# Kernel tuning notes

Measured on AMD Instinct MI355X. Metric: run time of the kernel, lower is better.

The kernel has to match this reference:

```python
import jax, jax.numpy as jnp
import numpy as np


def setup_inputs() -> dict:
    key = jax.random.key(0)
    k1, k2 = jax.random.split(key)
    x = jax.random.normal(k1, (4, 1, 16384), dtype=jnp.float32)  # [B, C, T]
    # dictionary initialized uniform(-1, 1) as in nn.Parameter(...).uniform_(-1, 1)
    d = jax.random.uniform(k2, (256, 1, 256), dtype=jnp.float32, minval=-1.0, maxval=1.0)  # [A, C, K]
    return {"x": x, "d": d, "n_iterations": 16}


def reference(x, d, n_iterations):
    B, C, T = x.shape
    A, _, K = d.shape
    pad = K // 2
    # normalize each atom over (channels, atom_size) dims, i.e. d_normalization_dims=(-1,-2)
    norms = jnp.linalg.norm(d.reshape(A, -1), axis=-1)
    dn = d / (norms[:, None, None] + 1e-12)

    # work in a padded domain so conv output position == start index in padded residual
    rp = jnp.pad(x, ((0, 0), (0, 0), (pad, pad)))        # residual, [B, C, T+2*pad]
    recon = jnp.zeros_like(rp)                            # accumulated reconstruction
    Tout = T + 2 * pad - K + 1                            # conv output length

    def step(carry, _):
        rp, recon = carry
        # cross-correlation of residual with every atom: [B, A, Tout]
        fm = jax.lax.conv_general_dilated(
            rp, dn, window_strides=(1,), padding='VALID',
            dimension_numbers=('NCH', 'OIH', 'NCH'))
        flat = fm.reshape(B, A * Tout)
        idx = jnp.argmax(flat, axis=-1)                   # signed max, per batch item
        val = jnp.take_along_axis(flat, idx[:, None], axis=-1)[:, 0]
        atom_idx = idx // Tout
        pos = idx % Tout                                  # start index in padded domain
        atoms = dn[atom_idx] * val[:, None, None]         # [B, C, K]

        def upd(r, rec, a, p):
            seg = jax.lax.dynamic_slice(r, (0, p), (C, K))
            r2 = jax.lax.dynamic_update_slice(r, seg - a, (0, p))
            segr = jax.lax.dynamic_slice(rec, (0, p), (C, K))
            rec2 = jax.lax.dynamic_update_slice(rec, segr + a, (0, p))
            return r2, rec2

        rp2, recon2 = jax.vmap(upd)(rp, recon, atoms, pos)
        return (rp2, recon2), None

    (rp, recon), _ = jax.lax.scan(step, (rp, recon), None, length=n_iterations)
    # crop padding -> reconstruction with same shape as x
    return recon[:, :, pad:pad + T]
```

## Files before the change

### kernel.cpp

```cpp
#include <hip/hip_runtime.h>
#include <hip/hip_cooperative_groups.h>
#include <math.h>

namespace cg = cooperative_groups;

#define B    4
#define T    16384
#define A    256
#define K    256
#define PAD  128
#define TP   (T + 2*PAD)
#define TOUT (TP - K + 1)
#define ITERS 16
#define CHUNK 512
#define NCHUNK 33
#define NCP  36
#define TILE 2048
#define NTILE 9
#define NBLK 512

struct Smem {
    float rp[TILE + K + 16];
    float dnA[K];
    float dnB[K];
    float dnsel[K];
    float wv[16]; int wi[16];
    float fv; int fi;
};

#define TAP(acc, s0,s1,s2,s3, dq) { acc = fmaf(s0,(dq).x,acc); acc = fmaf(s1,(dq).y,acc); \
                                    acc = fmaf(s2,(dq).z,acc); acc = fmaf(s3,(dq).w,acc); }

__device__ __forceinline__ void wave_amax(float& bv, int& bi) {
    #pragma unroll
    for (int off = 32; off; off >>= 1) {
        float ov = __shfl_down(bv, off);
        int   oi = __shfl_down(bi, off);
        if (ov > bv || (ov == bv && oi < bi)) { bv = ov; bi = oi; }
    }
}

__device__ __forceinline__ void gbar(unsigned* c, unsigned target) {
    __syncthreads();
    if (threadIdx.x == 0) {
        __hip_atomic_fetch_add(c, 1u, __ATOMIC_RELEASE, __HIP_MEMORY_SCOPE_AGENT);
        while (__hip_atomic_load(c, __ATOMIC_ACQUIRE, __HIP_MEMORY_SCOPE_AGENT) < target)
            __builtin_amdgcn_s_sleep(2);
    }
    __syncthreads();
}

__device__ __forceinline__ void dev_norm(int bid, int tid, const float* __restrict__ d,
                                         float* __restrict__ dn, Smem& sm) {
    if (bid < 128) {
        int lane = tid & 63, w = tid >> 6;
        #pragma unroll
        for (int s = 0; s < 2; s++) {
            int atom = (bid & 127)*2 + s;
            float v = d[atom*K + tid];
            float sq = v*v;
            #pragma unroll
            for (int off = 32; off; off >>= 1) sq += __shfl_down(sq, off);
            if (lane == 0) sm.wv[w] = sq;
            __syncthreads();
            float norm = sqrtf(sm.wv[0] + sm.wv[1] + sm.wv[2] + sm.wv[3]) + 1e-12f;
            dn[atom*K + tid] = v / norm;
            __syncthreads();
        }
    }
}

__device__ __forceinline__ void dev_init(int bid, int tid, const float* __restrict__ x,
                                         float* __restrict__ rp, float* __restrict__ recon) {
    for (int i = bid*256 + tid; i < B*TP; i += NBLK*256) {
        int bb = i / TP, t = i - bb*TP;
        float v = (t >= PAD && t < PAD + T) ? x[bb*T + (t - PAD)] : 0.f;
        rp[i] = v;
        recon[i] = 0.f;
    }
}

__device__ void dev_conv(int a0, int b, int tid, const float* __restrict__ rp,
                         const float* __restrict__ dn,
                         float* __restrict__ segval, int* __restrict__ segidx,
                         float* __restrict__ abv, int* __restrict__ abi, Smem& sm) {
    const int aA = a0*2, aB = a0*2 + 1;
    const int lane = tid & 63, w = tid >> 6;
    sm.dnA[tid] = dn[aA*K + tid];
    sm.dnB[tid] = dn[aB*K + tid];
    const float4* rp4 = (const float4*)(rp + (size_t)b*TP);

    for (int tile = 0; tile < NTILE; tile++) {
        int t0 = tile * TILE;
        __syncthreads();
        float4* s4 = (float4*)sm.rp;
        for (int i = tid; i < 580; i += 256) {
            int g = t0/4 + i;
            float4 v = {0.f,0.f,0.f,0.f};
            if (g*4 < TP) v = rp4[g];
            s4[i] = v;
        }
        __syncthreads();
        const float4* srp4 = (const float4*)sm.rp;
        const float4* dA4  = (const float4*)sm.dnA;
        const float4* dB4  = (const float4*)sm.dnB;
        float accA0[4] = {0,0,0,0}, accA1[4] = {0,0,0,0};
        float accB0[4] = {0,0,0,0}, accB1[4] = {0,0,0,0};
        float4 p = srp4[tid];
        float4 q = srp4[tid + 256];
        #pragma unroll 4
        for (int kq = 0; kq < 64; kq++) {
            float4 dA = dA4[kq];
            float4 dB = dB4[kq];
            float4 pn = srp4[tid + kq + 1];
            float4 qn = srp4[tid + 256 + kq + 1];
            TAP(accA0[0], p.x,p.y,p.z,p.w, dA); TAP(accA0[1], p.y,p.z,p.w,pn.x, dA);
            TAP(accA0[2], p.z,p.w,pn.x,pn.y, dA); TAP(accA0[3], p.w,pn.x,pn.y,pn.z, dA);
            TAP(accB0[0], p.x,p.y,p.z,p.w, dB); TAP(accB0[1], p.y,p.z,p.w,pn.x, dB);
            TAP(accB0[2], p.z,p.w,pn.x,pn.y, dB); TAP(accB0[3], p.w,pn.x,pn.y,pn.z, dB);
            TAP(accA1[0], q.x,q.y,q.z,q.w, dA); TAP(accA1[1], q.y,q.z,q.w,qn.x, dA);
            TAP(accA1[2], q.z,q.w,qn.x,qn.y, dA); TAP(accA1[3], q.w,qn.x,qn.y,qn.z, dA);
            TAP(accB1[0], q.x,q.y,q.z,q.w, dB); TAP(accB1[1], q.y,q.z,q.w,qn.x, dB);
            TAP(accB1[2], q.z,q.w,qn.x,qn.y, dB); TAP(accB1[3], q.w,qn.x,qn.y,qn.z, dB);
            p = pn; q = qn;
        }
        int lt = tid * 4;
        float bvA0 = -INFINITY, bvA1 = -INFINITY, bvB0 = -INFINITY, bvB1 = -INFINITY;
        int biA0 = 0x7fffffff, biA1 = 0x7fffffff, biB0 = 0x7fffffff, biB1 = 0x7fffffff;
        #pragma unroll
        for (int j = 0; j < 4; j++) {
            int t = t0 + lt + j;
            if (t < TOUT) {
                if (accA0[j] > bvA0) { bvA0 = accA0[j]; biA0 = aA*TOUT + t; }
                if (accB0[j] > bvB0) { bvB0 = accB0[j]; biB0 = aB*TOUT + t; }
            }
            int t1 = t0 + 1024 + lt + j;
            if (t1 < TOUT) {
                if (accA1[j] > bvA1) { bvA1 = accA1[j]; biA1 = aA*TOUT + t1; }
                if (accB1[j] > bvB1) { bvB1 = accB1[j]; biB1 = aB*TOUT + t1; }
            }
        }
        wave_amax(bvA0, biA0); wave_amax(bvA1, biA1);
        wave_amax(bvB0, biB0); wave_amax(bvB1, biB1);
        if (lane == 0) {
            sm.wv[w]    = bvA0; sm.wi[w]    = biA0;
            sm.wv[4+w]  = bvA1; sm.wi[4+w]  = biA1;
            sm.wv[8+w]  = bvB0; sm.wi[8+w]  = biB0;
            sm.wv[12+w] = bvB1; sm.wi[12+w] = biB1;
        }
        __syncthreads();
        if (tid < 4) {
            float v0 = sm.wv[2*tid];   int i0 = sm.wi[2*tid];
            float v1 = sm.wv[2*tid+1]; int i1 = sm.wi[2*tid+1];
            if (v1 > v0 || (v1 == v0 && i1 < i0)) { v0 = v1; i0 = i1; }
            int chunk = tile*4 + tid;
            if (chunk < NCHUNK) {
                segval[((size_t)b*A + aA)*NCP + chunk] = v0;
                segidx[((size_t)b*A + aA)*NCP + chunk] = i0;
            }
        } else if (tid >= 64 && tid < 68) {
            int c = tid - 64;
            float v0 = sm.wv[8+2*c];   int i0 = sm.wi[8+2*c];
            float v1 = sm.wv[8+2*c+1]; int i1 = sm.wi[8+2*c+1];
            if (v1 > v0 || (v1 == v0 && i1 < i0)) { v0 = v1; i0 = i1; }
            int chunk = tile*4 + c;
            if (chunk < NCHUNK) {
                segval[((size_t)b*A + aB)*NCP + chunk] = v0;
                segidx[((size_t)b*A + aB)*NCP + chunk] = i0;
            }
        }
    }
    __syncthreads();
    if (w < 2) {
        int atom = (w == 0) ? aA : aB;
        float bv = -INFINITY; int bi = 0x7fffffff;
        if (lane < NCHUNK) {
            bv = segval[((size_t)b*A + atom)*NCP + lane];
            bi = segidx[((size_t)b*A + atom)*NCP + lane];
        }
        wave_amax(bv, bi);
        if (lane == 0) { abv[b*A + atom] = bv; abi[b*A + atom] = bi; }
    }
}

__device__ void dev_iter(int a0, int b, int tid, int last,
                         const float* __restrict__ avc, const int* __restrict__ aic,
                         float* __restrict__ avn, int* __restrict__ ain,
                         const float* __restrict__ rin, float* __restrict__ rout,
                         float* __restrict__ recon, const float* __restrict__ dn,
                         float* __restrict__ segval, int* __restrict__ segidx, Smem& sm) {
    const int aA = a0*2, aB = a0*2 + 1;
    const int lane = tid & 63, w = tid >> 6;
    sm.dnA[tid] = dn[aA*K + tid];
    sm.dnB[tid] = dn[aB*K + tid];
    {
        float bv = avc[b*A + tid]; int bi = aic[b*A + tid];
        wave_amax(bv, bi);
        if (lane == 0) { sm.wv[w] = bv; sm.wi[w] = bi; }
        __syncthreads();
        if (tid == 0) {
            bv = sm.wv[0]; bi = sm.wi[0];
            for (int j = 1; j < 4; j++)
                if (sm.wv[j] > bv || (sm.wv[j] == bv && sm.wi[j] < bi)) { bv = sm.wv[j]; bi = sm.wi[j]; }
            sm.fv = bv; sm.fi = bi;
        }
        __syncthreads();
    }
    float val = sm.fv; int idx = sm.fi;
    int atom = idx / TOUT, pos = idx - atom*TOUT;
    sm.dnsel[tid] = dn[atom*K + tid];

    int lo = pos - (K-1); if (lo < 0) lo = 0;
    int c_lo = lo >> 9;
    int tbase = c_lo * CHUNK;

    if (!last) {
        const float4* rin4 = (const float4*)(rin + (size_t)b*TP);
        float4* s4 = (float4*)sm.rp;
        for (int i = tid; i < 324; i += 256) {
            int g = tbase/4 + i;
            float4 v = {0.f,0.f,0.f,0.f};
            if (g*4 < TP) v = rin4[g];
            s4[i] = v;
        }
    }
    __syncthreads();
    if (!last) {
        const float4* rin4 = (const float4*)(rin + (size_t)b*TP);
        float4* rout4 = (float4*)(rout + (size_t)b*TP);
        int i = a0*256 + tid;
        if (i < TP/4) {
            float4 v = rin4[i];
            int o = i*4 - pos;
            if (o > -4 && o < K) {
                if (o+0 >= 0 && o+0 < K) v.x -= val * sm.dnsel[o+0];
                if (o+1 >= 0 && o+1 < K) v.y -= val * sm.dnsel[o+1];
                if (o+2 >= 0 && o+2 < K) v.z -= val * sm.dnsel[o+2];
                if (o+3 >= 0 && o+3 < K) v.w -= val * sm.dnsel[o+3];
            }
            rout4[i] = v;
        }
    }
    if (a0 == 0) {
        recon[(size_t)b*TP + pos + tid] += val * sm.dnsel[tid];
    }
    if (last) return;

    sm.rp[pos + tid - tbase] -= val * sm.dnsel[tid];
    __syncthreads();

    const float4* srp4 = (const float4*)sm.rp;
    const float4* dA4  = (const float4*)sm.dnA;
    const float4* dB4  = (const float4*)sm.dnB;
    float cA[4] = {0,0,0,0}, cB[4] = {0,0,0,0};
    float4 p = srp4[tid];
    #pragma unroll 4
    for (int kq = 0; kq < 64; kq++) {
        float4 dA = dA4[kq];
        float4 dB = dB4[kq];
        float4 pn = srp4[tid + kq + 1];
        TAP(cA[0], p.x,p.y,p.z,p.w, dA); TAP(cA[1], p.y,p.z,p.w,pn.x, dA);
        TAP(cA[2], p.z,p.w,pn.x,pn.y, dA); TAP(cA[3], p.w,pn.x,pn.y,pn.z, dA);
        TAP(cB[0], p.x,p.y,p.z,p.w, dB); TAP(cB[1], p.y,p.z,p.w,pn.x, dB);
        TAP(cB[2], p.z,p.w,pn.x,pn.y, dB); TAP(cB[3], p.w,pn.x,pn.y,pn.z, dB);
        p = pn;
    }
    int lt = tid * 4;
    float bvA = -INFINITY, bvB = -INFINITY;
    int biA = 0x7fffffff, biB = 0x7fffffff;
    #pragma unroll
    for (int j = 0; j < 4; j++) {
        int t = tbase + lt + j;
        if (t < TOUT) {
            if (cA[j] > bvA) { bvA = cA[j]; biA = aA*TOUT + t; }
            if (cB[j] > bvB) { bvB = cB[j]; biB = aB*TOUT + t; }
        }
    }
    wave_amax(bvA, biA); wave_amax(bvB, biB);
    if (lane == 0) { sm.wv[w] = bvA; sm.wi[w] = biA; sm.wv[8+w] = bvB; sm.wi[8+w] = biB; }
    __syncthreads();
    if (tid < 2) {
        float v0 = sm.wv[2*tid];   int i0 = sm.wi[2*tid];
        float v1 = sm.wv[2*tid+1]; int i1 = sm.wi[2*tid+1];
        if (v1 > v0 || (v1 == v0 && i1 < i0)) { v0 = v1; i0 = i1; }
        int chunk = c_lo + tid;
        if (chunk < NCHUNK) {
            segval[((size_t)b*A + aA)*NCP + chunk] = v0;
            segidx[((size_t)b*A + aA)*NCP + chunk] = i0;
        }
    } else if (tid >= 64 && tid < 66) {
        int c = tid - 64;
        float v0 = sm.wv[8+2*c];   int i0 = sm.wi[8+2*c];
        float v1 = sm.wv[8+2*c+1]; int i1 = sm.wi[8+2*c+1];
        if (v1 > v0 || (v1 == v0 && i1 < i0)) { v0 = v1; i0 = i1; }
        int chunk = c_lo + c;
        if (chunk < NCHUNK) {
            segval[((size_t)b*A + aB)*NCP + chunk] = v0;
            segidx[((size_t)b*A + aB)*NCP + chunk] = i0;
        }
    }
    __syncthreads();
    if (w < 2) {
        int at = (w == 0) ? aA : aB;
        float bv = -INFINITY; int bi = 0x7fffffff;
        if (lane < NCHUNK) {
            bv = segval[((size_t)b*A + at)*NCP + lane];
            bi = segidx[((size_t)b*A + at)*NCP + lane];
        }
        wave_amax(bv, bi);
        if (lane == 0) { avn[b*A + at] = bv; ain[b*A + at] = bi; }
    }
}

__global__ void __launch_bounds__(256, 2)
k_coop(const float* __restrict__ x, const float* __restrict__ d, float* __restrict__ out,
       float* __restrict__ dn, float* __restrict__ rp0, float* __restrict__ rp1,
       float* __restrict__ recon, float* __restrict__ segval, int* __restrict__ segidx,
       float* __restrict__ abv0, int* __restrict__ abi0,
       float* __restrict__ abv1, int* __restrict__ abi1, unsigned* __restrict__ bar) {
    __shared__ Smem sm;
    const int bid = blockIdx.x, tid = threadIdx.x;
    const int a0 = bid & 127, b = bid >> 7;
    unsigned gen = 0;
    dev_norm(bid, tid, d, dn, sm);
    dev_init(bid, tid, x, rp0, recon);
    gen++; gbar(bar, gen*NBLK);
    dev_conv(a0, b, tid, rp0, dn, segval, segidx, abv0, abi0, sm);
    gen++; gbar(bar, gen*NBLK);
    const float* rin = rp0; float* rout = rp1;
    const float* avc = abv0; const int* aic = abi0;
    float* avn = abv1; int* ain = abi1;
    for (int it = 0; it < ITERS; it++) {
        dev_iter(a0, b, tid, it == ITERS-1, avc, aic, avn, ain,
                 rin, rout, recon, dn, segval, segidx, sm);
        { const float* t1 = rin; rin = rout; rout = (float*)t1; }
        { const float* t2 = avc; avc = avn; avn = (float*)t2; }
        { const int*   t3 = aic; aic = ain; ain = (int*)t3; }
        gen++; gbar(bar, gen*NBLK);
    }
    for (int i = bid*256 + tid; i < B*T; i += NBLK*256) {
        int bb = i / T, t = i - bb*T;
        out[i] = recon[(size_t)bb*TP + PAD + t];
    }
}

__global__ void __launch_bounds__(256) k_f_norm_init(const float* x, const float* d,
                                                     float* dn, float* rp0, float* recon) {
    __shared__ Smem sm;
    dev_norm(blockIdx.x, threadIdx.x, d, dn, sm);
    dev_init(blockIdx.x, threadIdx.x, x, rp0, recon);
}
__global__ void __launch_bounds__(256, 2) k_f_conv(const float* rp, const float* dn,
                                                   float* segval, int* segidx,
                                                   float* abv, int* abi) {
    __shared__ Smem sm;
    dev_conv(blockIdx.x & 127, blockIdx.x >> 7, threadIdx.x, rp, dn, segval, segidx, abv, abi, sm);
}
__global__ void __launch_bounds__(256, 2) k_f_iter(int last,
                                                   const float* avc, const int* aic,
                                                   float* avn, int* ain,
                                                   const float* rin, float* rout,
                                                   float* recon, const float* dn,
                                                   float* segval, int* segidx) {
    __shared__ Smem sm;
    dev_iter(blockIdx.x & 127, blockIdx.x >> 7, threadIdx.x, last,
             avc, aic, avn, ain, rin, rout, recon, dn, segval, segidx, sm);
}
__global__ void k_f_out(const float* recon, float* out) {
    int i = blockIdx.x * blockDim.x + threadIdx.x;
    if (i >= B*T) return;
    int b = i / T, t = i - b*T;
    out[i] = recon[(size_t)b*TP + PAD + t];
}

extern "C" void kernel_launch(void* const* d_in, const int* in_sizes, int n_in,
                              void* d_out, int out_size, void* d_ws, size_t ws_size,
                              hipStream_t stream) {
    const float* x = (const float*)d_in[0];
    const float* d = (const float*)d_in[1];
    float* out = (float*)d_out;

    float* ws     = (float*)d_ws;
    float* dn     = ws;
    float* rp0    = dn  + (size_t)A*K;
    float* rp1    = rp0 + (size_t)B*TP;
    float* recon  = rp1 + (size_t)B*TP;
    float* segval = recon + (size_t)B*TP;
    int*   segidx = (int*)(segval + (size_t)B*A*NCP);
    float* abv0   = (float*)(segidx + (size_t)B*A*NCP);
    float* abv1   = abv0 + (size_t)B*A;
    int*   abi0   = (int*)(abv1 + (size_t)B*A);
    int*   abi1   = abi0 + (size_t)B*A;
    unsigned* bar = (unsigned*)(abi1 + (size_t)B*A);

    int nb = 0, ncu = 0;
    hipError_t e1 = hipOccupancyMaxActiveBlocksPerMultiprocessor(&nb, (const void*)k_coop, 256, 0);
    hipError_t e2 = hipDeviceGetAttribute(&ncu, hipDeviceAttributeMultiprocessorCount, 0);
    bool coop = (e1 == hipSuccess && e2 == hipSuccess && nb > 0 && ncu > 0 &&
                 (long)nb * ncu >= NBLK);
    if (coop) {
        hipMemsetAsync(bar, 0, 64, stream);
        void* args[] = {(void*)&x, (void*)&d, (void*)&out, (void*)&dn,
                        (void*)&rp0, (void*)&rp1, (void*)&recon,
                        (void*)&segval, (void*)&segidx,
                        (void*)&abv0, (void*)&abi0, (void*)&abv1, (void*)&abi1,
                        (void*)&bar};
        hipError_t e = hipLaunchCooperativeKernel((const void*)k_coop, dim3(NBLK), dim3(256),
                                                  args, 0, stream);
        if (e == hipSuccess) return;
    }
    k_f_norm_init<<<NBLK, 256, 0, stream>>>(x, d, dn, rp0, recon);
    k_f_conv<<<NBLK, 256, 0, stream>>>(rp0, dn, segval, segidx, abv0, abi0);
    float* rbuf[2] = {rp0, rp1};
    float* av[2]   = {abv0, abv1};
    int*   ai[2]   = {abi0, abi1};
    for (int it = 0; it < ITERS; it++) {
        k_f_iter<<<NBLK, 256, 0, stream>>>(it == ITERS-1 ? 1 : 0,
                                           av[it & 1], ai[it & 1],
                                           av[(it + 1) & 1], ai[(it + 1) & 1],
                                           rbuf[it & 1], rbuf[(it + 1) & 1],
                                           recon, dn, segval, segidx);
    }
    k_f_out<<<(B*T + 255)/256, 256, 0, stream>>>(recon, out);
}
```

Before: 547.3 us.

## Double block size, split grid barrier per batch, and widen iter recompute window

Blocks grow from 256 to 512 threads, each thread now computing one output strip instead of two, so each block has twice the waves with fewer registers per thread. The single global barrier becomes one barrier counter per batch item, so each batch synchronises only its own 128 blocks. The normalisation and init phase is restructured around this per-batch partition, and each iteration's local re-convolution now covers four aligned chunks instead of two. The intent is more latency hiding and less barrier contention, at the cost of recomputing a wider window each iteration and a higher residency requirement for the cooperative launch.

```diff
diff --git a/kernel.cpp b/kernel.cpp
--- a/kernel.cpp
+++ b/kernel.cpp
@@ -1,8 +1,6 @@
 #include <hip/hip_runtime.h>
 #include <hip/hip_cooperative_groups.h>
 #include <math.h>
-
-namespace cg = cooperative_groups;
 
 #define B    4
 #define T    16384
@@ -18,11 +16,12 @@
 #define TILE 2048
 #define NTILE 9
 #define NBLK 512
+#define BTH  512
+#define NBB  128
 
 struct Smem {
-    float rp[TILE + K + 16];
-    float dnA[K];
-    float dnB[K];
+    float rp[2336];
+    float dnAB[2*K];
     float dnsel[K];
     float wv[16]; int wi[16];
     float fv; int fi;
@@ -50,33 +49,28 @@
     __syncthreads();
 }
 
-__device__ __forceinline__ void dev_norm(int bid, int tid, const float* __restrict__ d,
-                                         float* __restrict__ dn, Smem& sm) {
-    if (bid < 128) {
-        int lane = tid & 63, w = tid >> 6;
-        #pragma unroll
-        for (int s = 0; s < 2; s++) {
-            int atom = (bid & 127)*2 + s;
-            float v = d[atom*K + tid];
-            float sq = v*v;
-            #pragma unroll
-            for (int off = 32; off; off >>= 1) sq += __shfl_down(sq, off);
-            if (lane == 0) sm.wv[w] = sq;
-            __syncthreads();
-            float norm = sqrtf(sm.wv[0] + sm.wv[1] + sm.wv[2] + sm.wv[3]) + 1e-12f;
-            dn[atom*K + tid] = v / norm;
-            __syncthreads();
-        }
-    }
-}
-
-__device__ __forceinline__ void dev_init(int bid, int tid, const float* __restrict__ x,
-                                         float* __restrict__ rp, float* __restrict__ recon) {
-    for (int i = bid*256 + tid; i < B*TP; i += NBLK*256) {
-        int bb = i / TP, t = i - bb*TP;
-        float v = (t >= PAD && t < PAD + T) ? x[bb*T + (t - PAD)] : 0.f;
-        rp[i] = v;
-        recon[i] = 0.f;
+__device__ __forceinline__ void dev_norm_init(int a0, int b, int tid,
+                                              const float* __restrict__ x,
+                                              const float* __restrict__ d,
+                                              float* __restrict__ dn,
+                                              float* __restrict__ rp,
+                                              float* __restrict__ recon, Smem& sm) {
+    int lane = tid & 63, w = tid >> 6;
+    int half = tid >> 8, k = tid & 255;
+    int atom = a0*2 + half;
+    float v = d[atom*K + k];
+    float sq = v*v;
+    #pragma unroll
+    for (int off = 32; off; off >>= 1) sq += __shfl_down(sq, off);
+    if (lane == 0) sm.wv[w] = sq;
+    __syncthreads();
+    float norm = sqrtf(sm.wv[half*4] + sm.wv[half*4+1] + sm.wv[half*4+2] + sm.wv[half*4+3]) + 1e-12f;
+    dn[atom*K + k] = v / norm;
+    __syncthreads();
+    for (int i = a0*BTH + tid; i < TP; i += NBB*BTH) {
+        float xv = (i >= PAD && i < PAD + T) ? x[b*T + (i - PAD)] : 0.f;
+        rp[(size_t)b*TP + i] = xv;
+        recon[(size_t)b*TP + i] = 0.f;
     }
 }
 
@@ -84,17 +78,16 @@
                          const float* __restrict__ dn,
                          float* __restrict__ segval, int* __restrict__ segidx,
                          float* __restrict__ abv, int* __restrict__ abi, Smem& sm) {
-    const int aA = a0*2, aB = a0*2 + 1;
+    const int aA = a0*2, aB = aA + 1;
     const int lane = tid & 63, w = tid >> 6;
-    sm.dnA[tid] = dn[aA*K + tid];
-    sm.dnB[tid] = dn[aB*K + tid];
+    sm.dnAB[tid] = dn[aA*K + tid];
     const float4* rp4 = (const float4*)(rp + (size_t)b*TP);
 
     for (int tile = 0; tile < NTILE; tile++) {
         int t0 = tile * TILE;
         __syncthreads();
         float4* s4 = (float4*)sm.rp;
-        for (int i = tid; i < 580; i += 256) {
+        for (int i = tid; i < 580; i += BTH) {
             int g = t0/4 + i;
             float4 v = {0.f,0.f,0.f,0.f};
             if (g*4 < TP) v = rp4[g];
@@ -102,52 +95,34 @@
         }
         __syncthreads();
         const float4* srp4 = (const float4*)sm.rp;
-        const float4* dA4  = (const float4*)sm.dnA;
-        const float4* dB4  = (const float4*)sm.dnB;
-        float accA0[4] = {0,0,0,0}, accA1[4] = {0,0,0,0};
-        float accB0[4] = {0,0,0,0}, accB1[4] = {0,0,0,0};
+        const float4* dA4  = (const float4*)sm.dnAB;
+        const float4* dB4  = dA4 + 64;
+        float accA[4] = {0,0,0,0}, accB[4] = {0,0,0,0};
         float4 p = srp4[tid];
-        float4 q = srp4[tid + 256];
         #pragma unroll 4
         for (int kq = 0; kq < 64; kq++) {
             float4 dA = dA4[kq];
             float4 dB = dB4[kq];
             float4 pn = srp4[tid + kq + 1];
-            float4 qn = srp4[tid + 256 + kq + 1];
-            TAP(accA0[0], p.x,p.y,p.z,p.w, dA); TAP(accA0[1], p.y,p.z,p.w,pn.x, dA);
-            TAP(accA0[2], p.z,p.w,pn.x,pn.y, dA); TAP(accA0[3], p.w,pn.x,pn.y,pn.z, dA);
-            TAP(accB0[0], p.x,p.y,p.z,p.w, dB); TAP(accB0[1], p.y,p.z,p.w,pn.x, dB);
-            TAP(accB0[2], p.z,p.w,pn.x,pn.y, dB); TAP(accB0[3], p.w,pn.x,pn.y,pn.z, dB);
-            TAP(accA1[0], q.x,q.y,q.z,q.w, dA); TAP(accA1[1], q.y,q.z,q.w,qn.x, dA);
-            TAP(accA1[2], q.z,q.w,qn.x,qn.y, dA); TAP(accA1[3], q.w,qn.x,qn.y,qn.z, dA);
-            TAP(accB1[0], q.x,q.y,q.z,q.w, dB); TAP(accB1[1], q.y,q.z,q.w,qn.x, dB);
-            TAP(accB1[2], q.z,q.w,qn.x,qn.y, dB); TAP(accB1[3], q.w,qn.x,qn.y,qn.z, dB);
-            p = pn; q = qn;
+            TAP(accA[0], p.x,p.y,p.z,p.w, dA); TAP(accA[1], p.y,p.z,p.w,pn.x, dA);
+            TAP(accA[2], p.z,p.w,pn.x,pn.y, dA); TAP(accA[3], p.w,pn.x,pn.y,pn.z, dA);
+            TAP(accB[0], p.x,p.y,p.z,p.w, dB); TAP(accB[1], p.y,p.z,p.w,pn.x, dB);
+            TAP(accB[2], p.z,p.w,pn.x,pn.y, dB); TAP(accB[3], p.w,pn.x,pn.y,pn.z, dB);
+            p = pn;
         }
         int lt = tid * 4;
-        float bvA0 = -INFINITY, bvA1 = -INFINITY, bvB0 = -INFINITY, bvB1 = -INFINITY;
-        int biA0 = 0x7fffffff, biA1 = 0x7fffffff, biB0 = 0x7fffffff, biB1 = 0x7fffffff;
+        float bvA = -INFINITY, bvB = -INFINITY;
+        int biA = 0x7fffffff, biB = 0x7fffffff;
         #pragma unroll
         for (int j = 0; j < 4; j++) {
             int t = t0 + lt + j;
             if (t < TOUT) {
-                if (accA0[j] > bvA0) { bvA0 = accA0[j]; biA0 = aA*TOUT + t; }
-                if (accB0[j] > bvB0) { bvB0 = accB0[j]; biB0 = aB*TOUT + t; }
+                if (accA[j] > bvA) { bvA = accA[j]; biA = aA*TOUT + t; }
+                if (accB[j] > bvB) { bvB = accB[j]; biB = aB*TOUT + t; }
             }
-            int t1 = t0 + 1024 + lt + j;
-            if (t1 < TOUT) {
-                if (accA1[j] > bvA1) { bvA1 = accA1[j]; biA1 = aA*TOUT + t1; }
-                if (accB1[j] > bvB1) { bvB1 = accB1[j]; biB1 = aB*TOUT + t1; }
-            }
-        }
-        wave_amax(bvA0, biA0); wave_amax(bvA1, biA1);
-        wave_amax(bvB0, biB0); wave_amax(bvB1, biB1);
-        if (lane == 0) {
-            sm.wv[w]    = bvA0; sm.wi[w]    = biA0;
-            sm.wv[4+w]  = bvA1; sm.wi[4+w]  = biA1;
-            sm.wv[8+w]  = bvB0; sm.wi[8+w]  = biB0;
-            sm.wv[12+w] = bvB1; sm.wi[12+w] = biB1;
-        }
+        }
+        wave_amax(bvA, biA); wave_amax(bvB, biB);
+        if (lane == 0) { sm.wv[w] = bvA; sm.wi[w] = biA; sm.wv[8+w] = bvB; sm.wi[8+w] = biB; }
         __syncthreads();
         if (tid < 4) {
             float v0 = sm.wv[2*tid];   int i0 = sm.wi[2*tid];
@@ -189,18 +164,17 @@
                          const float* __restrict__ rin, float* __restrict__ rout,
                          float* __restrict__ recon, const float* __restrict__ dn,
                          float* __restrict__ segval, int* __restrict__ segidx, Smem& sm) {
-    const int aA = a0*2, aB = a0*2 + 1;
+    const int aA = a0*2, aB = aA + 1;
     const int lane = tid & 63, w = tid >> 6;
-    sm.dnA[tid] = dn[aA*K + tid];
-    sm.dnB[tid] = dn[aB*K + tid];
     {
-        float bv = avc[b*A + tid]; int bi = aic[b*A + tid];
+        float bv = avc[b*A + (tid & 255)];
+        int   bi = aic[b*A + (tid & 255)];
         wave_amax(bv, bi);
         if (lane == 0) { sm.wv[w] = bv; sm.wi[w] = bi; }
         __syncthreads();
         if (tid == 0) {
             bv = sm.wv[0]; bi = sm.wi[0];
-            for (int j = 1; j < 4; j++)
+            for (int j = 1; j < 8; j++)
                 if (sm.wv[j] > bv || (sm.wv[j] == bv && sm.wi[j] < bi)) { bv = sm.wv[j]; bi = sm.wi[j]; }
             sm.fv = bv; sm.fi = bi;
         }
@@ -208,16 +182,17 @@
     }
     float val = sm.fv; int idx = sm.fi;
     int atom = idx / TOUT, pos = idx - atom*TOUT;
-    sm.dnsel[tid] = dn[atom*K + tid];
+    if (tid < K) sm.dnsel[tid] = dn[atom*K + tid];
+    sm.dnAB[tid] = dn[aA*K + tid];
 
     int lo = pos - (K-1); if (lo < 0) lo = 0;
-    int c_lo = lo >> 9;
-    int tbase = c_lo * CHUNK;
+    int c_base = (lo >> 9) & ~1;
+    int tbase = c_base * CHUNK;
 
     if (!last) {
         const float4* rin4 = (const float4*)(rin + (size_t)b*TP);
         float4* s4 = (float4*)sm.rp;
-        for (int i = tid; i < 324; i += 256) {
+        for (int i = tid; i < 580; i += BTH) {
             int g = tbase/4 + i;
             float4 v = {0.f,0.f,0.f,0.f};
             if (g*4 < TP) v = rin4[g];
@@ -228,7 +203,7 @@
     if (!last) {
         const float4* rin4 = (const float4*)(rin + (size_t)b*TP);
         float4* rout4 = (float4*)(rout + (size_t)b*TP);
-        int i = a0*256 + tid;
+        int i = a0*BTH + tid;
         if (i < TP/4) {
             float4 v = rin4[i];
             int o = i*4 - pos;
@@ -241,28 +216,26 @@
             rout4[i] = v;
         }
     }
-    if (a0 == 0) {
-        recon[(size_t)b*TP + pos + tid] += val * sm.dnsel[tid];
-    }
+    if (a0 == 0 && tid < K) recon[(size_t)b*TP + pos + tid] += val * sm.dnsel[tid];
     if (last) return;
 
-    sm.rp[pos + tid - tbase] -= val * sm.dnsel[tid];
+    if (tid < K) sm.rp[pos - tbase + tid] -= val * sm.dnsel[tid];
     __syncthreads();
 
     const float4* srp4 = (const float4*)sm.rp;
-    const float4* dA4  = (const float4*)sm.dnA;
-    const float4* dB4  = (const float4*)sm.dnB;
-    float cA[4] = {0,0,0,0}, cB[4] = {0,0,0,0};
+    const float4* dA4  = (const float4*)sm.dnAB;
+    const float4* dB4  = dA4 + 64;
+    float accA[4] = {0,0,0,0}, accB[4] = {0,0,0,0};
     float4 p = srp4[tid];
     #pragma unroll 4
     for (int kq = 0; kq < 64; kq++) {
         float4 dA = dA4[kq];
         float4 dB = dB4[kq];
         float4 pn = srp4[tid + kq + 1];
-        TAP(cA[0], p.x,p.y,p.z,p.w, dA); TAP(cA[1], p.y,p.z,p.w,pn.x, dA);
-        TAP(cA[2], p.z,p.w,pn.x,pn.y, dA); TAP(cA[3], p.w,pn.x,pn.y,pn.z, dA);
-        TAP(cB[0], p.x,p.y,p.z,p.w, dB); TAP(cB[1], p.y,p.z,p.w,pn.x, dB);
-        TAP(cB[2], p.z,p.w,pn.x,pn.y, dB); TAP(cB[3], p.w,pn.x,pn.y,pn.z, dB);
+        TAP(accA[0], p.x,p.y,p.z,p.w, dA); TAP(accA[1], p.y,p.z,p.w,pn.x, dA);
+        TAP(accA[2], p.z,p.w,pn.x,pn.y, dA); TAP(accA[3], p.w,pn.x,pn.y,pn.z, dA);
+        TAP(accB[0], p.x,p.y,p.z,p.w, dB); TAP(accB[1], p.y,p.z,p.w,pn.x, dB);
+        TAP(accB[2], p.z,p.w,pn.x,pn.y, dB); TAP(accB[3], p.w,pn.x,pn.y,pn.z, dB);
         p = pn;
     }
     int lt = tid * 4;
@@ -272,28 +245,28 @@
     for (int j = 0; j < 4; j++) {
         int t = tbase + lt + j;
         if (t < TOUT) {
-            if (cA[j] > bvA) { bvA = cA[j]; biA = aA*TOUT + t; }
-            if (cB[j] > bvB) { bvB = cB[j]; biB = aB*TOUT + t; }
+            if (accA[j] > bvA) { bvA = accA[j]; biA = aA*TOUT + t; }
+            if (accB[j] > bvB) { bvB = accB[j]; biB = aB*TOUT + t; }
         }
     }
     wave_amax(bvA, biA); wave_amax(bvB, biB);
     if (lane == 0) { sm.wv[w] = bvA; sm.wi[w] = biA; sm.wv[8+w] = bvB; sm.wi[8+w] = biB; }
     __syncthreads();
-    if (tid < 2) {
+    if (tid < 4) {
         float v0 = sm.wv[2*tid];   int i0 = sm.wi[2*tid];
         float v1 = sm.wv[2*tid+1]; int i1 = sm.wi[2*tid+1];
         if (v1 > v0 || (v1 == v0 && i1 < i0)) { v0 = v1; i0 = i1; }
-        int chunk = c_lo + tid;
+        int chunk = c_base + tid;
         if (chunk < NCHUNK) {
             segval[((size_t)b*A + aA)*NCP + chunk] = v0;
             segidx[((size_t)b*A + aA)*NCP + chunk] = i0;
         }
-    } else if (tid >= 64 && tid < 66) {
+    } else if (tid >= 64 && tid < 68) {
         int c = tid - 64;
         float v0 = sm.wv[8+2*c];   int i0 = sm.wi[8+2*c];
         float v1 = sm.wv[8+2*c+1]; int i1 = sm.wi[8+2*c+1];
         if (v1 > v0 || (v1 == v0 && i1 < i0)) { v0 = v1; i0 = i1; }
-        int chunk = c_lo + c;
+        int chunk = c_base + c;
         if (chunk < NCHUNK) {
             segval[((size_t)b*A + aB)*NCP + chunk] = v0;
             segidx[((size_t)b*A + aB)*NCP + chunk] = i0;
@@ -312,7 +285,7 @@
     }
 }
 
-__global__ void __launch_bounds__(256, 2)
+__global__ void __launch_bounds__(BTH, 4)
 k_coop(const float* __restrict__ x, const float* __restrict__ d, float* __restrict__ out,
        float* __restrict__ dn, float* __restrict__ rp0, float* __restrict__ rp1,
        float* __restrict__ recon, float* __restrict__ segval, int* __restrict__ segidx,
@@ -320,13 +293,13 @@
        float* __restrict__ abv1, int* __restrict__ abi1, unsigned* __restrict__ bar) {
     __shared__ Smem sm;
     const int bid = blockIdx.x, tid = threadIdx.x;
-    const int a0 = bid & 127, b = bid >> 7;
+    const int a0 = bid & (NBB-1), b = bid >> 7;
+    unsigned* bar_b = bar + b*256;
     unsigned gen = 0;
-    dev_norm(bid, tid, d, dn, sm);
-    dev_init(bid, tid, x, rp0, recon);
-    gen++; gbar(bar, gen*NBLK);
+    dev_norm_init(a0, b, tid, x, d, dn, rp0, recon, sm);
+    gen++; gbar(bar_b, gen*NBB);
     dev_conv(a0, b, tid, rp0, dn, segval, segidx, abv0, abi0, sm);
-    gen++; gbar(bar, gen*NBLK);
+    gen++; gbar(bar_b, gen*NBB);
     const float* rin = rp0; float* rout = rp1;
     const float* avc = abv0; const int* aic = abi0;
     float* avn = abv1; int* ain = abi1;
@@ -336,34 +309,31 @@
         { const float* t1 = rin; rin = rout; rout = (float*)t1; }
         { const float* t2 = avc; avc = avn; avn = (float*)t2; }
         { const int*   t3 = aic; aic = ain; ain = (int*)t3; }
-        gen++; gbar(bar, gen*NBLK);
-    }
-    for (int i = bid*256 + tid; i < B*T; i += NBLK*256) {
-        int bb = i / T, t = i - bb*T;
-        out[i] = recon[(size_t)bb*TP + PAD + t];
-    }
-}
-
-__global__ void __launch_bounds__(256) k_f_norm_init(const float* x, const float* d,
+        gen++; gbar(bar_b, gen*NBB);
+    }
+    for (int i = a0*BTH + tid; i < T; i += NBB*BTH)
+        out[b*T + i] = recon[(size_t)b*TP + PAD + i];
+}
+
+__global__ void __launch_bounds__(BTH) k_f_norm_init(const float* x, const float* d,
                                                      float* dn, float* rp0, float* recon) {
     __shared__ Smem sm;
-    dev_norm(blockIdx.x, threadIdx.x, d, dn, sm);
-    dev_init(blockIdx.x, threadIdx.x, x, rp0, recon);
-}
-__global__ void __launch_bounds__(256, 2) k_f_conv(const float* rp, const float* dn,
+    dev_norm_init(blockIdx.x & (NBB-1), blockIdx.x >> 7, threadIdx.x, x, d, dn, rp0, recon, sm);
+}
+__global__ void __launch_bounds__(BTH, 4) k_f_conv(const float* rp, const float* dn,
                                                    float* segval, int* segidx,
                                                    float* abv, int* abi) {
     __shared__ Smem sm;
-    dev_conv(blockIdx.x & 127, blockIdx.x >> 7, threadIdx.x, rp, dn, segval, segidx, abv, abi, sm);
-}
-__global__ void __launch_bounds__(256, 2) k_f_iter(int last,
+    dev_conv(blockIdx.x & (NBB-1), blockIdx.x >> 7, threadIdx.x, rp, dn, segval, segidx, abv, abi, sm);
+}
+__global__ void __launch_bounds__(BTH, 4) k_f_iter(int last,
                                                    const float* avc, const int* aic,
                                                    float* avn, int* ain,
                                                    const float* rin, float* rout,
                                                    float* recon, const float* dn,
                                                    float* segval, int* segidx) {
     __shared__ Smem sm;
-    dev_iter(blockIdx.x & 127, blockIdx.x >> 7, threadIdx.x, last,
+    dev_iter(blockIdx.x & (NBB-1), blockIdx.x >> 7, threadIdx.x, last,
              avc, aic, avn, ain, rin, rout, recon, dn, segval, segidx, sm);
 }
 __global__ void k_f_out(const float* recon, float* out) {
@@ -394,28 +364,28 @@
     unsigned* bar = (unsigned*)(abi1 + (size_t)B*A);
 
     int nb = 0, ncu = 0;
-    hipError_t e1 = hipOccupancyMaxActiveBlocksPerMultiprocessor(&nb, (const void*)k_coop, 256, 0);
+    hipError_t e1 = hipOccupancyMaxActiveBlocksPerMultiprocessor(&nb, (const void*)k_coop, BTH, 0);
     hipError_t e2 = hipDeviceGetAttribute(&ncu, hipDeviceAttributeMultiprocessorCount, 0);
     bool coop = (e1 == hipSuccess && e2 == hipSuccess && nb > 0 && ncu > 0 &&
                  (long)nb * ncu >= NBLK);
     if (coop) {
-        hipMemsetAsync(bar, 0, 64, stream);
+        hipMemsetAsync(bar, 0, 4*256*sizeof(unsigned), stream);
         void* args[] = {(void*)&x, (void*)&d, (void*)&out, (void*)&dn,
                         (void*)&rp0, (void*)&rp1, (void*)&recon,
                         (void*)&segval, (void*)&segidx,
                         (void*)&abv0, (void*)&abi0, (void*)&abv1, (void*)&abi1,
                         (void*)&bar};
-        hipError_t e = hipLaunchCooperativeKernel((const void*)k_coop, dim3(NBLK), dim3(256),
+        hipError_t e = hipLaunchCooperativeKernel((const void*)k_coop, dim3(NBLK), dim3(BTH),
                                                   args, 0, stream);
         if (e == hipSuccess) return;
     }
-    k_f_norm_init<<<NBLK, 256, 0, stream>>>(x, d, dn, rp0, recon);
-    k_f_conv<<<NBLK, 256, 0, stream>>>(rp0, dn, segval, segidx, abv0, abi0);
+    k_f_norm_init<<<NBLK, BTH, 0, stream>>>(x, d, dn, rp0, recon);
+    k_f_conv<<<NBLK, BTH, 0, stream>>>(rp0, dn, segval, segidx, abv0, abi0);
     float* rbuf[2] = {rp0, rp1};
     float* av[2]   = {abv0, abv1};
     int*   ai[2]   = {abi0, abi1};
     for (int it = 0; it < ITERS; it++) {
-        k_f_iter<<<NBLK, 256, 0, stream>>>(it == ITERS-1 ? 1 : 0,
+        k_f_iter<<<NBLK, BTH, 0, stream>>>(it == ITERS-1 ? 1 : 0,
                                            av[it & 1], ai[it & 1],
                                            av[(it + 1) & 1], ai[(it + 1) & 1],
                                            rbuf[it & 1], rbuf[(it + 1) & 1],
```

After: 727.6 us. 1.33x slower.
